# Kernel tuning notes

Hardware: AMD Instinct MI355X
Metric: run time of the kernel (lower is better)

The kernel has to match this reference:

```python
import jax, jax.numpy as jnp
import numpy as np

ZERO = 1e-8
L = 2            # num_gnn_layers
D = 256          # dim_node_features
B = 32           # graphs per batch
NPG = 256        # nodes per graph
N = B * NPG      # total nodes
E = 131072       # edges per edge-type
MAX_TOKENS = 256 # MAX_TOKENS_OF_A_POST
UPD = 0.5        # args.updated_weights_for_A


def _make_edges(k):
    k1, k2, k3 = jax.random.split(k, 3)
    g = jax.random.randint(k1, (E,), 0, B) * NPG          # keep edges within a graph
    src = g + jax.random.randint(k2, (E,), 0, NPG)
    dst = g + jax.random.randint(k3, (E,), 0, NPG)
    return jnp.stack([src, dst]).astype(jnp.int64)


def setup_inputs() -> dict:
    key = jax.random.key(0)
    ks = jax.random.split(key, 12)
    x = jax.random.normal(ks[0], (N, D), dtype=jnp.float32)
    ei_e = _make_edges(ks[1]); ew_e = jax.random.uniform(ks[2], (E,), dtype=jnp.float32)
    ei_p = _make_edges(ks[3]); ew_p = jax.random.uniform(ks[4], (E,), dtype=jnp.float32)
    ei_o = _make_edges(ks[5]); ew_o = jax.random.uniform(ks[6], (E,), dtype=jnp.float32)
    entity_mask = jax.random.randint(ks[7], (B, NPG), 0, 2).astype(bool)
    pattern_mask = jax.random.randint(ks[8], (B, NPG), 0, 2).astype(bool)
    s = 1.0 / np.sqrt(D)
    W_gcn = (jax.random.normal(ks[9], (L, 3, D, D), dtype=jnp.float32) * s)
    b_gcn = jnp.zeros((L, 3, D), dtype=jnp.float32)
    T_dyn = (jax.random.normal(ks[10], (L, D, D), dtype=jnp.float32) * s)
    return {
        'x': x,
        'edge_index_entity': ei_e, 'edge_weight_entity': ew_e,
        'edge_index_pattern': ei_p, 'edge_weight_pattern': ew_p,
        'edge_index_others': ei_o, 'edge_weight_others': ew_o,
        'entity_mask': entity_mask, 'pattern_mask': pattern_mask,
        'W_gcn': W_gcn, 'b_gcn': b_gcn, 'T_dyn': T_dyn,
    }


def _normalized_correlation_matrix(H):
    # cosine-similarity correlation matrix, symmetrically degree-normalized
    nrm = jnp.sqrt(jnp.sum(H * H, axis=1))
    A = (H @ H.T) / (nrm[:, None] * nrm[None, :] + ZERO)
    dinv = 1.0 / jnp.sqrt(jnp.abs(jnp.sum(A, axis=1)) + ZERO)
    return dinv[:, None] * A * dinv[None, :]


def _gcn(H, W, b, ei, ew):
    # GCNConv(add_self_loops=False, normalize=False): scatter-sum of weighted source messages
    msg = (H @ W)[ei[0]] * ew[:, None]                     # [E, D]
    return jax.ops.segment_sum(msg, ei[1], num_segments=N) + b


def _forward(x, we0, wp0, wo0, W_gcn, b_gcn, T_dyn,
             ei_e, ei_p, ei_o, entity_mask, pattern_mask):
    H = x
    A = _normalized_correlation_matrix(H)                  # [N, N]
    for i in range(L):
        if i == 0:
            we, wp, wo = we0, wp0, wo0
        else:
            # diag(one_hot(src) @ A @ one_hot(dst).T) == A[src, dst]
            we = A[ei_e[0], ei_e[1]]
            wp = A[ei_p[0], ei_p[1]]
            wo = A[ei_o[0], ei_o[1]]
        He = _gcn(H, W_gcn[i, 0], b_gcn[i, 0], ei_e, we)
        Hp = _gcn(H, W_gcn[i, 1], b_gcn[i, 1], ei_p, wp)
        Ho = _gcn(H, W_gcn[i, 2], b_gcn[i, 2], ei_o, wo)
        H = jax.nn.relu(He + Hp + Ho)
        A_hat = jax.nn.sigmoid((H @ T_dyn[i]) @ H.T)
        A = (1.0 - UPD) * A + UPD * A_hat
    # per-graph diagonal blocks of A  -> [B, NPG, NPG]
    A4 = A.reshape(B, NPG, B, NPG)
    idx = jnp.arange(B)
    blocks = A4[idx, :, idx, :]
    A_sum = jnp.sum(blocks, axis=-1)                       # [B, NPG]
    ent_cols = jnp.einsum('bij,bj->bi', blocks, entity_mask.astype(A.dtype))
    pat_cols = jnp.einsum('bij,bj->bi', blocks, pattern_mask.astype(A.dtype))
    map_pattern = A_sum - ent_cols
    map_entity = A_sum - pat_cols

    def finish(m):
        mn = jnp.min(m, axis=1, keepdims=True)
        mx = jnp.max(m, axis=1, keepdims=True)
        m = (m - mn) / (mx - mn + ZERO)
        m = m / (jnp.sum(m, axis=1, keepdims=True) + ZERO)
        return m[:, :MAX_TOKENS]                           # padding() with NPG==MAX_TOKENS

    return finish(map_entity), finish(map_pattern)


def reference(x, edge_index_entity, edge_weight_entity,
              edge_index_pattern, edge_weight_pattern,
              edge_index_others, edge_weight_others,
              entity_mask, pattern_mask, W_gcn, b_gcn, T_dyn):
    return _forward(x, edge_weight_entity, edge_weight_pattern, edge_weight_others,
                    W_gcn, b_gcn, T_dyn,
                    edge_index_entity, edge_index_pattern, edge_index_others,
                    entity_mask, pattern_mask)
```

## Files before the change

### kernel.cpp

```cpp
#include <hip/hip_runtime.h>

#define NND   8192
#define DDIM  256
#define NGRP  32
#define ZEROF 1e-8f
#define LSTR  40
#define TSTR  72
#define OFF_AH 0
#define OFF_AL 2560
#define OFF_BH 5120
#define OFF_BL 10240
#define OFF_TT 5120
#define LDS_U16 16384

typedef unsigned short u16;
typedef __attribute__((ext_vector_type(8))) short short8v;
typedef __attribute__((ext_vector_type(4))) float float4v;

__device__ inline u16 f2bf(float x) {
  unsigned u = __float_as_uint(x);
  u += 0x7fffu + ((u >> 16) & 1u);
  return (u16)(u >> 16);
}
__device__ inline float bf2f(u16 h) { return __uint_as_float((unsigned)h << 16); }
__device__ inline void split2(float x, u16& h, u16& l) {
  h = f2bf(x);
  l = f2bf(x - bf2f(h));
}

__device__ inline float wave_sum(float v) {
#pragma unroll
  for (int off = 32; off > 0; off >>= 1) v += __shfl_down(v, off, 64);
  return v;
}

#define LOAD_REGS(tt, kk)                                                                   \
  {                                                                                         \
    int m_ = tid >> 2, kq_ = (tid & 3) * 8;                                                 \
    size_t aoff_;                                                                           \
    if (MODE == 1)                                                                          \
      aoff_ = (size_t)((tt) * 256 + bym * 64 + m_) * 8192 + (size_t)(g * 256 + (kk) + kq_); \
    else if (MODE == 2 || MODE == 3)                                                        \
      aoff_ = (size_t)(g * 256 + bym * 64 + m_) * 256 + (kk) + kq_;                         \
    else                                                                                    \
      aoff_ = (size_t)(bym * 64 + m_) * 256 + (kk) + kq_;                                   \
    rAh = *(const short8v*)&Ah_g[aoff_];                                                    \
    rAl = *(const short8v*)&Al_g[aoff_];                                                    \
    if (MODE == 1) {                                                                        \
      int n_ = tid >> 2, kq2_ = (tid & 3) * 8;                                              \
      const float* pb_ = Bfp + (((size_t)g * 3 + (tt)) << 16) +                             \
                         (size_t)(col0 + n_) * 256 + (kk) + kq2_;                           \
      rBf[0] = *(const float4*)pb_;                                                         \
      rBf[1] = *(const float4*)(pb_ + 4);                                                   \
    } else if (HALF) {                                                                      \
      int n_ = tid & 63, kq2_ = (tid >> 6) * 8;                                             \
      size_t boff_ = (size_t)(((MODE == 2 || MODE == 3) ? g * 256 : 0) + col0 + n_) * 256   \
                     + (kk) + kq2_;                                                         \
      rBh0 = *(const short8v*)&Bh_g[boff_];                                                 \
      rBl0 = *(const short8v*)&Bl_g[boff_];                                                 \
    } else {                                                                                \
      int n_ = tid & 127, kq2_ = (tid >> 7) * 16;                                           \
      size_t boff_ = (size_t)(col0 + n_) * 256 + (kk) + kq2_;                               \
      rBh0 = *(const short8v*)&Bh_g[boff_]; rBh1 = *(const short8v*)&Bh_g[boff_ + 8];       \
      rBl0 = *(const short8v*)&Bl_g[boff_]; rBl1 = *(const short8v*)&Bl_g[boff_ + 8];       \
    }                                                                                       \
  }

template<int MODE, bool HALF>
__device__ __forceinline__ void mfma_body(
    u16* lds,
    const u16* __restrict__ Ah_g, const u16* __restrict__ Al_g,
    const u16* __restrict__ Bh_g, const u16* __restrict__ Bl_g,
    const float* __restrict__ Bfp,
    float* __restrict__ Cf, u16* __restrict__ Ch, u16* __restrict__ Cl,
    const float* __restrict__ nrm, const float* __restrict__ dinv,
    const float* __restrict__ bias,
    int bxm, int bym, int g) {
  u16* Ahs = lds + OFF_AH;
  u16* Als = lds + OFF_AL;
  u16* Bhs = lds + OFF_BH;
  u16* Bls = lds + OFF_BL;
  u16* Tt  = lds + OFF_TT;
  const int NJ = HALF ? 2 : 4;
  const int tid = threadIdx.x;
  const int col0 = bxm * (HALF ? 64 : 128);
  const int w = tid >> 6, lane = tid & 63;
  const int lm = lane & 15, lq = lane >> 4;
  const int wr = (w >> 1) * 32, wc = (w & 1) * (HALF ? 32 : 64);

  float4v acc[2][4];
#pragma unroll
  for (int i = 0; i < 2; ++i)
#pragma unroll
    for (int j = 0; j < NJ; ++j) acc[i][j] = (float4v)0.f;

  short8v rAh, rAl, rBh0, rBh1, rBl0, rBl1;
  float4 rBf[2];
  const int TOTAL = (MODE == 1) ? 24 : 8;

  LOAD_REGS(0, 0);
  for (int step = 0; step < TOTAL; ++step) {
    if (step) __syncthreads();
    {
      int m = tid >> 2, kq = (tid & 3) * 8;
      *(short8v*)&Ahs[m * LSTR + kq] = rAh;
      *(short8v*)&Als[m * LSTR + kq] = rAl;
    }
    if (MODE == 1) {
      int n = tid >> 2, kq2 = (tid & 3) * 8;
      u16 hh[8], ll[8];
      split2(rBf[0].x, hh[0], ll[0]); split2(rBf[0].y, hh[1], ll[1]);
      split2(rBf[0].z, hh[2], ll[2]); split2(rBf[0].w, hh[3], ll[3]);
      split2(rBf[1].x, hh[4], ll[4]); split2(rBf[1].y, hh[5], ll[5]);
      split2(rBf[1].z, hh[6], ll[6]); split2(rBf[1].w, hh[7], ll[7]);
      *(short8v*)&Bhs[n * LSTR + kq2] = *(short8v*)hh;
      *(short8v*)&Bls[n * LSTR + kq2] = *(short8v*)ll;
    } else if (HALF) {
      int n = tid & 63, kq2 = (tid >> 6) * 8;
      *(short8v*)&Bhs[n * LSTR + kq2] = rBh0;
      *(short8v*)&Bls[n * LSTR + kq2] = rBl0;
    } else {
      int n = tid & 127, kq2 = (tid >> 7) * 16;
      *(short8v*)&Bhs[n * LSTR + kq2] = rBh0; *(short8v*)&Bhs[n * LSTR + kq2 + 8] = rBh1;
      *(short8v*)&Bls[n * LSTR + kq2] = rBl0; *(short8v*)&Bls[n * LSTR + kq2 + 8] = rBl1;
    }
    __syncthreads();
    int nxt = step + 1;
    if (nxt < TOTAL) {
      int tt = nxt >> 3, kk = (nxt & 7) * 32;
      LOAD_REGS(tt, kk);
    }
    short8v ah[2], al[2], bh[4], bl[4];
#pragma unroll
    for (int i = 0; i < 2; ++i) {
      int r = wr + i * 16 + lm;
      ah[i] = *(const short8v*)&Ahs[r * LSTR + lq * 8];
      al[i] = *(const short8v*)&Als[r * LSTR + lq * 8];
    }
#pragma unroll
    for (int j = 0; j < NJ; ++j) {
      int r = wc + j * 16 + lm;
      bh[j] = *(const short8v*)&Bhs[r * LSTR + lq * 8];
      bl[j] = *(const short8v*)&Bls[r * LSTR + lq * 8];
    }
#pragma unroll
    for (int i = 0; i < 2; ++i)
#pragma unroll
      for (int j = 0; j < NJ; ++j) {
        acc[i][j] = __builtin_amdgcn_mfma_f32_16x16x32_bf16(ah[i], bh[j], acc[i][j], 0, 0, 0);
        acc[i][j] = __builtin_amdgcn_mfma_f32_16x16x32_bf16(ah[i], bl[j], acc[i][j], 0, 0, 0);
        acc[i][j] = __builtin_amdgcn_mfma_f32_16x16x32_bf16(al[i], bh[j], acc[i][j], 0, 0, 0);
      }
  }

  if (MODE == 2 || MODE == 3) {
#pragma unroll
    for (int i = 0; i < 2; ++i) {
#pragma unroll
      for (int r = 0; r < 4; ++r) {
        int grow = g * 256 + bym * 64 + wr + i * 16 + lq * 4 + r;
        float di = 0.f, ni = 0.f;
        if (MODE == 2) { di = dinv[grow]; ni = nrm[grow]; }
#pragma unroll
        for (int j = 0; j < NJ; ++j) {
          int gcol = col0 + wc + j * 16 + lm;
          size_t ci = (size_t)grow * 256 + gcol;
          float v = acc[i][j][r];
          if (MODE == 2) {
            int gj = g * 256 + gcol;
            Cf[ci] = v * di * dinv[gj] / (ni * nrm[gj] + ZEROF);
          } else {
            Cf[ci] = 0.5f * Cf[ci] + 0.5f * (1.f / (1.f + expf(-v)));
          }
        }
      }
    }
  } else {
    float bsum[8];
    if (MODE == 1) {
#pragma unroll
      for (int i = 0; i < 2; ++i)
#pragma unroll
        for (int r = 0; r < 4; ++r) {
          int d = bym * 64 + wr + i * 16 + lq * 4 + r;
          bsum[i * 4 + r] = bias[d] + bias[256 + d] + bias[512 + d];
        }
    }
    u16 hv[32], lv[32];
#pragma unroll
    for (int i = 0; i < 2; ++i)
#pragma unroll
      for (int j = 0; j < NJ; ++j)
#pragma unroll
        for (int r = 0; r < 4; ++r) {
          float v = acc[i][j][r];
          if (MODE == 1) v = fmaxf(v + bsum[i * 4 + r], 0.f);
          split2(v, hv[(i * 4 + r) * NJ + j], lv[(i * 4 + r) * NJ + j]);
        }
    int ebase1 = (MODE == 1) ? (g * 256 + col0) : col0;
    int ebase2 = bym * 64;
    size_t estride = (MODE == 0) ? 8192 : 256;
#pragma unroll
    for (int ph = 0; ph < 2; ++ph) {
      __syncthreads();
      const u16* sv = ph ? lv : hv;
#pragma unroll
      for (int i = 0; i < 2; ++i)
#pragma unroll
        for (int j = 0; j < NJ; ++j)
#pragma unroll
          for (int r = 0; r < 4; ++r)
            Tt[(wc + j * 16 + lm) * TSTR + wr + i * 16 + lq * 4 + r] = sv[(i * 4 + r) * NJ + j];
      __syncthreads();
      u16* dst = ph ? Cl : Ch;
      int cc0 = tid >> 3, mm0 = (tid & 7) * 8;
#pragma unroll
      for (int it = 0; it < (HALF ? 2 : 4); ++it) {
        int cc = it * 32 + cc0;
        short8v v = *(const short8v*)&Tt[cc * TSTR + mm0];
        *(short8v*)&dst[(size_t)(ebase1 + cc) * estride + ebase2 + mm0] = v;
      }
    }
  }
}

__global__ void k_prep(const int* __restrict__ e0, const int* __restrict__ e1,
                       const int* __restrict__ e2, const unsigned char* __restrict__ m0,
                       const unsigned char* __restrict__ m1,
                       const float* __restrict__ W, const float* __restrict__ T,
                       const float* __restrict__ x,
                       const float* __restrict__ ew0, const float* __restrict__ ew1,
                       const float* __restrict__ ew2,
                       float* __restrict__ emf, float* __restrict__ pmf,
                       u16* __restrict__ Wth, u16* __restrict__ Wtl,
                       u16* __restrict__ sct, uint2* __restrict__ recs,
                       float* __restrict__ nrm, float* __restrict__ Spart,
                       u16* __restrict__ Hh, u16* __restrict__ Hl,
                       int E_, int nCvt, int nBkt) {
  __shared__ float tile[32][33];
  __shared__ float inv[64];
  __shared__ int nz[1];
  __shared__ unsigned int hcnt[768];
  __shared__ unsigned int hoff[768];
  __shared__ unsigned int ppart[256];
  __shared__ uint2 stage[768];
  const int b = blockIdx.x, tid = threadIdx.x;
  if (b < nCvt) {
    if (tid == 0) nz[0] = 0;
    __syncthreads();
    int i4 = tid * 4;
    int c = (m0[i4 + 1] != 0) + (m0[i4 + 2] != 0) + (m0[i4 + 3] != 0);
    if (c) atomicAdd(&nz[0], c);
    __syncthreads();
    int fM = (nz[0] == 0);
    int i = b * 256 + tid;
    if (i < NND) {
      unsigned char v = fM ? m0[4 * i] : m0[i];
      emf[i] = 1.f - (float)(v != 0);
    } else {
      int j = i - NND;
      unsigned char v = fM ? m1[4 * j] : m1[j];
      pmf[j] = 1.f - (float)(v != 0);
    }
  } else if (b < nCvt + nBkt) {
    if (tid == 0) nz[0] = 0;
    hcnt[tid] = 0; hcnt[tid + 256] = 0; hcnt[tid + 512] = 0;
    __syncthreads();
    if (e0[2 * tid + 1] != 0) atomicAdd(&nz[0], 1);
    __syncthreads();
    int fE = (nz[0] == 0);
    int e = (b - nCvt) * 256 + tid;
    bool valid = (e < E_);
    int mybid[3]; unsigned int myrec[3]; float myw[3];
    if (valid) {
#pragma unroll
      for (int t = 0; t < 3; ++t) {
        const int* ei = (t == 0) ? e0 : ((t == 1) ? e1 : e2);
        int src = fE ? ei[2 * e] : ei[e];
        int dst = fE ? ei[2 * (E_ + e)] : ei[E_ + e];
        int g = src >> 8, s = src & 255, d = dst & 255;
        mybid[t] = ((g * 3 + t) << 3) | (d >> 5);
        myrec[t] = (unsigned)(((d & 31) << 8) | s);
        myw[t] = (t == 0 ? ew0 : (t == 1 ? ew1 : ew2))[e];
        atomicAdd(&hcnt[mybid[t]], 1u);
      }
    }
    __syncthreads();
    unsigned c0 = hcnt[3 * tid], c1 = hcnt[3 * tid + 1], c2 = hcnt[3 * tid + 2];
    unsigned tsum = c0 + c1 + c2;
    ppart[tid] = tsum;
    __syncthreads();
    for (int off = 1; off < 256; off <<= 1) {
      unsigned v = (tid >= off) ? ppart[tid - off] : 0u;
      __syncthreads();
      ppart[tid] += v;
      __syncthreads();
    }
    unsigned base = ppart[tid] - tsum;
    hoff[3 * tid] = base;
    hoff[3 * tid + 1] = base + c0;
    hoff[3 * tid + 2] = base + c0 + c1;
    __syncthreads();
#pragma unroll
    for (int k = 0; k < 3; ++k) {
      int bin = tid + k * 256;
      unsigned cc = hcnt[bin]; if (cc > 31u) cc = 31u;
      sct[(size_t)(b - nCvt) * 768 + bin] = (u16)(hoff[bin] | (cc << 11));
    }
    __syncthreads();
    if (valid) {
#pragma unroll
      for (int t = 0; t < 3; ++t) {
        unsigned slot = atomicAdd(&hoff[mybid[t]], 1u);
        stage[slot] = make_uint2(myrec[t], __float_as_uint(myw[t]));
      }
    }
    __syncthreads();
    uint2* dstp = &recs[(size_t)(b - nCvt) * 768];
    dstp[tid] = stage[tid];
    dstp[tid + 256] = stage[tid + 256];
    dstp[tid + 512] = stage[tid + 512];
  } else if (b < nCvt + nBkt + 512) {
    int bb = b - nCvt - nBkt;
    int mat = bb >> 6, rem = bb & 63;
    int k0 = (rem >> 3) * 32, n0 = (rem & 7) * 32;
    const float* src = (mat < 6) ? (W + (size_t)mat * 65536) : (T + (size_t)(mat - 6) * 65536);
    int r = tid >> 3, c4 = (tid & 7) * 4;
    const float4 v = *(const float4*)&src[(size_t)(k0 + r) * 256 + n0 + c4];
    tile[r][c4 + 0] = v.x; tile[r][c4 + 1] = v.y; tile[r][c4 + 2] = v.z; tile[r][c4 + 3] = v.w;
    __syncthreads();
    float o[4] = {tile[c4 + 0][r], tile[c4 + 1][r], tile[c4 + 2][r], tile[c4 + 3][r]};
    u16 hh[4], ll[4];
#pragma unroll
    for (int q = 0; q < 4; ++q) split2(o[q], hh[q], ll[q]);
    size_t off = (size_t)mat * 65536 + (size_t)(n0 + r) * 256 + k0 + c4;
    *(ushort4*)&Wth[off] = *(ushort4*)hh;
    *(ushort4*)&Wtl[off] = *(ushort4*)ll;
  } else {
    int bn = b - nCvt - nBkt - 512;
    int n0 = bn * 64;
    int w = tid >> 6, lane = tid & 63;
    for (int it = 0; it < 16; ++it) {
      int nl = it * 4 + w;
      int node = n0 + nl;
      const float4 v = *(const float4*)&x[(size_t)node * 256 + lane * 4];
      u16 hh[4], ll[4];
      split2(v.x, hh[0], ll[0]); split2(v.y, hh[1], ll[1]);
      split2(v.z, hh[2], ll[2]); split2(v.w, hh[3], ll[3]);
      *(ushort4*)&Hh[(size_t)node * 256 + lane * 4] = *(ushort4*)hh;
      *(ushort4*)&Hl[(size_t)node * 256 + lane * 4] = *(ushort4*)ll;
      float s = wave_sum(v.x * v.x + v.y * v.y + v.z * v.z + v.w * v.w);
      if (lane == 0) { float nr = sqrtf(s); nrm[node] = nr; inv[nl] = 1.f / nr; }
    }
    __syncthreads();
    float s = 0.f;
    for (int i = 0; i < 64; ++i) s += x[(size_t)(n0 + i) * 256 + tid] * inv[i];
    Spart[bn * 256 + tid] = s;
  }
}

__global__ __launch_bounds__(256, 2) void k_stageA(
    const u16* __restrict__ Hinh, const u16* __restrict__ Hinl,
    const u16* __restrict__ Wth, const u16* __restrict__ Wtl, int l,
    u16* __restrict__ XWTh, u16* __restrict__ XWTl,
    const u16* __restrict__ sct, const uint2* __restrict__ recs, int nBkt,
    const float* __restrict__ Abuf, float* __restrict__ Mb,
    const float* __restrict__ x, const float* __restrict__ Spart,
    const float* __restrict__ nrm, float* __restrict__ dinv) {
  __shared__ u16 lds[LDS_U16];
  const int b = blockIdx.x;
  if (b < 768) {
    mfma_body<0, false>(lds, Hinh, Hinl, Wth + (size_t)l * 768 * 256,
                        Wtl + (size_t)l * 768 * 256, nullptr,
                        nullptr, XWTh, XWTl, nullptr, nullptr, nullptr,
                        b >> 7, b & 127, 0);
  } else if (b < 1536) {
    const int tid = threadIdx.x;
    int bid = b - 768;
    int gt = bid >> 3, chunk = bid & 7;
    int g = gt / 3;
    float* tile = (float*)lds;
    float4 z = make_float4(0.f, 0.f, 0.f, 0.f);
#pragma unroll
    for (int k = 0; k < 8; ++k) ((float4*)tile)[k * 256 + tid] = z;
    __syncthreads();
    for (int bb = tid; bb < nBkt; bb += 256) {
      unsigned sc = sct[(size_t)bb * 768 + bid];
      unsigned start = sc & 2047u, cnt = sc >> 11;
      const uint2* rp = &recs[(size_t)bb * 768 + start];
      for (unsigned k = 0; k < cnt; ++k) {
        uint2 r = rp[k];
        int s = r.x & 255, d5 = (r.x >> 8) & 31;
        float w = l ? Abuf[(size_t)(g * 256 + s) * 256 + chunk * 32 + d5]
                    : __uint_as_float(r.y);
        atomicAdd(&tile[d5 * 256 + s], w);
      }
    }
    __syncthreads();
    float4* dst = (float4*)&Mb[((size_t)gt << 16) + ((size_t)chunk << 13)];
#pragma unroll
    for (int k = 0; k < 8; ++k) dst[k * 256 + tid] = ((float4*)tile)[k * 256 + tid];
  } else {
    float* Sl = (float*)lds;
    const int tid = threadIdx.x;
    float s = 0.f;
    for (int bb = 0; bb < 128; ++bb) s += Spart[bb * 256 + tid];
    Sl[tid] = s;
    __syncthreads();
    int base = (b - 1536) * 64;
    int w = tid >> 6, lane = tid & 63;
    const float4 sv = *(const float4*)&Sl[lane * 4];
    for (int it = 0; it < 16; ++it) {
      int node = base + it * 4 + w;
      const float4 v = *(const float4*)&x[(size_t)node * 256 + lane * 4];
      float s2 = wave_sum(v.x * sv.x + v.y * sv.y + v.z * sv.z + v.w * sv.w);
      if (lane == 0) {
        float rowsum = s2 / nrm[node];
        dinv[node] = rsqrtf(fabsf(rowsum) + ZEROF);
      }
    }
  }
}

__global__ __launch_bounds__(256, 2) void k_stageB(
    const u16* __restrict__ XWTh, const u16* __restrict__ XWTl,
    const float* __restrict__ Mb,
    u16* __restrict__ Houth, u16* __restrict__ Houtl, const float* __restrict__ bias,
    const u16* __restrict__ xh, const u16* __restrict__ xl, float* __restrict__ Abuf,
    const float* __restrict__ nrm, const float* __restrict__ dinv) {
  __shared__ u16 lds[LDS_U16];
  const int b = blockIdx.x;
  if (b < 512) {
    int g = b & 31, r = b >> 5;
    mfma_body<1, true>(lds, XWTh, XWTl, nullptr, nullptr, Mb,
                       nullptr, Houth, Houtl, nullptr, nullptr, bias,
                       r >> 2, r & 3, g);
  } else {
    int bb = b - 512;
    int g = bb & 31, r = bb >> 5;
    mfma_body<2, true>(lds, xh, xl, xh, xl, nullptr, Abuf, nullptr, nullptr,
                       nrm, dinv, nullptr, r >> 2, r & 3, g);
  }
}

__global__ __launch_bounds__(256, 2) void k_stageC(
    const u16* __restrict__ Wth, const u16* __restrict__ Wtl, int l,
    const u16* __restrict__ Hh, const u16* __restrict__ Hl,
    u16* __restrict__ tmph, u16* __restrict__ tmpl) {
  __shared__ u16 lds[LDS_U16];
  const int b = blockIdx.x;
  mfma_body<4, true>(lds, Wth + (size_t)(6 + l) * 65536, Wtl + (size_t)(6 + l) * 65536,
                     Hh, Hl, nullptr, nullptr, tmph, tmpl, nullptr, nullptr, nullptr,
                     b & 127, b >> 7, 0);
}

__global__ __launch_bounds__(256, 2) void k_stageD(
    const u16* __restrict__ tmph, const u16* __restrict__ tmpl,
    const u16* __restrict__ Hh, const u16* __restrict__ Hl,
    float* __restrict__ Abuf) {
  __shared__ u16 lds[LDS_U16];
  const int b = blockIdx.x;
  int g = b & 31, r = b >> 5;
  mfma_body<3, true>(lds, tmph, tmpl, Hh, Hl, nullptr, Abuf, nullptr, nullptr,
                     nullptr, nullptr, nullptr, r >> 2, r & 3, g);
}

__global__ void k_maps(const float* __restrict__ Abuf, const float* __restrict__ emf,
                       const float* __restrict__ pmf, float* __restrict__ out) {
  __shared__ float sme[256], smp[256], red[256];
  const int g = blockIdx.x, tid = threadIdx.x, w = tid >> 6, lane = tid & 63;
  const int j0 = g * 256 + lane * 4;
  const float4 pmv = *(const float4*)&pmf[j0];
  const float4 emv = *(const float4*)&emf[j0];
  for (int it = 0; it < 64; ++it) {
    int nl = it * 4 + w;
    const float4 a = *(const float4*)&Abuf[((size_t)g * 256 + nl) * 256 + lane * 4];
    float me = a.x * pmv.x + a.y * pmv.y + a.z * pmv.z + a.w * pmv.w;
    float mp = a.x * emv.x + a.y * emv.y + a.z * emv.z + a.w * emv.w;
#pragma unroll
    for (int off = 32; off > 0; off >>= 1) {
      me += __shfl_down(me, off, 64);
      mp += __shfl_down(mp, off, 64);
    }
    if (lane == 0) { sme[nl] = me; smp[nl] = mp; }
  }
  __syncthreads();
  for (int which = 0; which < 2; ++which) {
    float v = which ? smp[tid] : sme[tid];
    red[tid] = v; __syncthreads();
    for (int s = 128; s > 0; s >>= 1) { if (tid < s) red[tid] = fminf(red[tid], red[tid + s]); __syncthreads(); }
    float mn = red[0]; __syncthreads();
    red[tid] = v; __syncthreads();
    for (int s = 128; s > 0; s >>= 1) { if (tid < s) red[tid] = fmaxf(red[tid], red[tid + s]); __syncthreads(); }
    float mx = red[0]; __syncthreads();
    float m = (v - mn) / (mx - mn + ZEROF);
    red[tid] = m; __syncthreads();
    for (int s = 128; s > 0; s >>= 1) { if (tid < s) red[tid] += red[tid + s]; __syncthreads(); }
    float sum = red[0]; __syncthreads();
    out[which * NND + g * 256 + tid] = m / (sum + ZEROF);
  }
}

extern "C" void kernel_launch(void* const* d_in, const int* in_sizes, int n_in,
                              void* d_out, int out_size, void* d_ws, size_t ws_size,
                              hipStream_t stream) {
  const float* x = (const float*)d_in[0];
  const unsigned char* em_raw = (const unsigned char*)d_in[7];
  const unsigned char* pm_raw = (const unsigned char*)d_in[8];
  const float* W  = (const float*)d_in[9];
  const float* bg = (const float*)d_in[10];
  const float* T  = (const float*)d_in[11];
  float* out = (float*)d_out;
  const int E_ = in_sizes[2];

  const int nCvt = (2 * NND) / 256;
  const int nBkt = (E_ + 255) / 256;

  float* ws = (float*)d_ws;
  size_t o = 0;
  float* Abuf = ws + o; o += (size_t)NND * 256;
  float* Mb3  = ws + o; o += (size_t)2 * NGRP * 3 * 65536;
  u16* Hh   = (u16*)(ws + o); o += (size_t)NND * 256 / 2;
  u16* Hl   = (u16*)(ws + o); o += (size_t)NND * 256 / 2;
  u16* H2h  = (u16*)(ws + o); o += (size_t)NND * 256 / 2;
  u16* H2l  = (u16*)(ws + o); o += (size_t)NND * 256 / 2;
  u16* tmph = (u16*)(ws + o); o += (size_t)NND * 256 / 2;
  u16* tmpl = (u16*)(ws + o); o += (size_t)NND * 256 / 2;
  u16* XWTh = (u16*)(ws + o); o += (size_t)768 * NND / 2;
  u16* XWTl = (u16*)(ws + o); o += (size_t)768 * NND / 2;
  u16* Wth  = (u16*)(ws + o); o += (size_t)8 * 65536 / 2;
  u16* Wtl  = (u16*)(ws + o); o += (size_t)8 * 65536 / 2;
  float* nrm   = ws + o; o += NND;
  float* dinv  = ws + o; o += NND;
  float* Spart = ws + o; o += 128 * 256;
  float* emf   = ws + o; o += NND;
  float* pmf   = ws + o; o += NND;
  u16* sct     = (u16*)(ws + o); o += (size_t)nBkt * 768 / 2;
  uint2* recs  = (uint2*)(ws + o); o += (size_t)nBkt * 768 * 2;

  const float* ew0 = (const float*)d_in[2];
  const float* ew1 = (const float*)d_in[4];
  const float* ew2 = (const float*)d_in[6];
  float* Mb_l0 = Mb3;
  float* Mb_l1 = Mb3 + (size_t)NGRP * 3 * 65536;

  k_prep<<<nCvt + nBkt + 512 + 128, 256, 0, stream>>>(
      (const int*)d_in[1], (const int*)d_in[3], (const int*)d_in[5], em_raw, pm_raw,
      W, T, x, ew0, ew1, ew2, emf, pmf, Wth, Wtl, sct, recs,
      nrm, Spart, Hh, Hl, E_, nCvt, nBkt);

  k_stageA<<<1664, 256, 0, stream>>>(Hh, Hl, Wth, Wtl, 0, XWTh, XWTl,
                                     sct, recs, nBkt, Abuf, Mb_l0,
                                     x, Spart, nrm, dinv);
  k_stageB<<<1024, 256, 0, stream>>>(XWTh, XWTl, Mb_l0, H2h, H2l, bg,
                                     Hh, Hl, Abuf, nrm, dinv);
  k_stageC<<<512, 256, 0, stream>>>(Wth, Wtl, 0, H2h, H2l, tmph, tmpl);
  k_stageD<<<512, 256, 0, stream>>>(tmph, tmpl, H2h, H2l, Abuf);

  k_stageA<<<1536, 256, 0, stream>>>(H2h, H2l, Wth, Wtl, 1, XWTh, XWTl,
                                     sct, recs, nBkt, Abuf, Mb_l1,
                                     x, Spart, nrm, dinv);
  k_stageB<<<512, 256, 0, stream>>>(XWTh, XWTl, Mb_l1, Hh, Hl, bg + 768,
                                    nullptr, nullptr, nullptr, nullptr, nullptr);
  k_stageC<<<512, 256, 0, stream>>>(Wth, Wtl, 1, Hh, Hl, tmph, tmpl);
  k_stageD<<<512, 256, 0, stream>>>(tmph, tmpl, Hh, Hl, Abuf);

  k_maps<<<NGRP, 256, 0, stream>>>(Abuf, emf, pmf, out);
}
```

Measured before the change: 275.3 us.

## Store scatter matrices as bf16 hi/lo split and widen stage-B GEMM tiles

```diff
diff --git a/kernel.cpp b/kernel.cpp
--- a/kernel.cpp
+++ b/kernel.cpp
@@ -46,21 +46,16 @@
       aoff_ = (size_t)(bym * 64 + m_) * 256 + (kk) + kq_;                                   \
     rAh = *(const short8v*)&Ah_g[aoff_];                                                    \
     rAl = *(const short8v*)&Al_g[aoff_];                                                    \
-    if (MODE == 1) {                                                                        \
-      int n_ = tid >> 2, kq2_ = (tid & 3) * 8;                                              \
-      const float* pb_ = Bfp + (((size_t)g * 3 + (tt)) << 16) +                             \
-                         (size_t)(col0 + n_) * 256 + (kk) + kq2_;                           \
-      rBf[0] = *(const float4*)pb_;                                                         \
-      rBf[1] = *(const float4*)(pb_ + 4);                                                   \
-    } else if (HALF) {                                                                      \
+    size_t bbase_ = (MODE == 1) ? ((size_t)(g * 3 + (tt)) << 16)                            \
+                  : ((MODE == 2 || MODE == 3) ? ((size_t)g << 16) : (size_t)0);             \
+    if (HALF) {                                                                             \
       int n_ = tid & 63, kq2_ = (tid >> 6) * 8;                                             \
-      size_t boff_ = (size_t)(((MODE == 2 || MODE == 3) ? g * 256 : 0) + col0 + n_) * 256   \
-                     + (kk) + kq2_;                                                         \
+      size_t boff_ = bbase_ + (size_t)(col0 + n_) * 256 + (kk) + kq2_;                      \
       rBh0 = *(const short8v*)&Bh_g[boff_];                                                 \
       rBl0 = *(const short8v*)&Bl_g[boff_];                                                 \
     } else {                                                                                \
       int n_ = tid & 127, kq2_ = (tid >> 7) * 16;                                           \
-      size_t boff_ = (size_t)(col0 + n_) * 256 + (kk) + kq2_;                               \
+      size_t boff_ = bbase_ + (size_t)(col0 + n_) * 256 + (kk) + kq2_;                      \
       rBh0 = *(const short8v*)&Bh_g[boff_]; rBh1 = *(const short8v*)&Bh_g[boff_ + 8];       \
       rBl0 = *(const short8v*)&Bl_g[boff_]; rBl1 = *(const short8v*)&Bl_g[boff_ + 8];       \
     }                                                                                       \
@@ -71,7 +66,6 @@
     u16* lds,
     const u16* __restrict__ Ah_g, const u16* __restrict__ Al_g,
     const u16* __restrict__ Bh_g, const u16* __restrict__ Bl_g,
-    const float* __restrict__ Bfp,
     float* __restrict__ Cf, u16* __restrict__ Ch, u16* __restrict__ Cl,
     const float* __restrict__ nrm, const float* __restrict__ dinv,
     const float* __restrict__ bias,
@@ -95,7 +89,6 @@
     for (int j = 0; j < NJ; ++j) acc[i][j] = (float4v)0.f;
 
   short8v rAh, rAl, rBh0, rBh1, rBl0, rBl1;
-  float4 rBf[2];
   const int TOTAL = (MODE == 1) ? 24 : 8;
 
   LOAD_REGS(0, 0);
@@ -106,16 +99,7 @@
       *(short8v*)&Ahs[m * LSTR + kq] = rAh;
       *(short8v*)&Als[m * LSTR + kq] = rAl;
     }
-    if (MODE == 1) {
-      int n = tid >> 2, kq2 = (tid & 3) * 8;
-      u16 hh[8], ll[8];
-      split2(rBf[0].x, hh[0], ll[0]); split2(rBf[0].y, hh[1], ll[1]);
-      split2(rBf[0].z, hh[2], ll[2]); split2(rBf[0].w, hh[3], ll[3]);
-      split2(rBf[1].x, hh[4], ll[4]); split2(rBf[1].y, hh[5], ll[5]);
-      split2(rBf[1].z, hh[6], ll[6]); split2(rBf[1].w, hh[7], ll[7]);
-      *(short8v*)&Bhs[n * LSTR + kq2] = *(short8v*)hh;
-      *(short8v*)&Bls[n * LSTR + kq2] = *(short8v*)ll;
-    } else if (HALF) {
+    if (HALF) {
       int n = tid & 63, kq2 = (tid >> 6) * 8;
       *(short8v*)&Bhs[n * LSTR + kq2] = rBh0;
       *(short8v*)&Bls[n * LSTR + kq2] = rBl0;
@@ -359,27 +343,29 @@
   }
 }
 
-__global__ __launch_bounds__(256, 2) void k_stageA(
+__global__ __launch_bounds__(256, 2) void k_gemmA(
     const u16* __restrict__ Hinh, const u16* __restrict__ Hinl,
     const u16* __restrict__ Wth, const u16* __restrict__ Wtl, int l,
-    u16* __restrict__ XWTh, u16* __restrict__ XWTl,
+    u16* __restrict__ XWTh, u16* __restrict__ XWTl) {
+  __shared__ u16 lds[LDS_U16];
+  const int b = blockIdx.x;
+  mfma_body<0, false>(lds, Hinh, Hinl, Wth + (size_t)l * 768 * 256,
+                      Wtl + (size_t)l * 768 * 256,
+                      nullptr, XWTh, XWTl, nullptr, nullptr, nullptr,
+                      b >> 7, b & 127, 0);
+}
+
+__global__ __launch_bounds__(256, 2) void k_mbuild(
     const u16* __restrict__ sct, const uint2* __restrict__ recs, int nBkt,
-    const float* __restrict__ Abuf, float* __restrict__ Mb,
+    const float* __restrict__ Abuf, u16* __restrict__ Mbh, u16* __restrict__ Mbl, int l,
     const float* __restrict__ x, const float* __restrict__ Spart,
     const float* __restrict__ nrm, float* __restrict__ dinv) {
-  __shared__ u16 lds[LDS_U16];
-  const int b = blockIdx.x;
+  __shared__ float tile[8192];
+  const int b = blockIdx.x, tid = threadIdx.x;
   if (b < 768) {
-    mfma_body<0, false>(lds, Hinh, Hinl, Wth + (size_t)l * 768 * 256,
-                        Wtl + (size_t)l * 768 * 256, nullptr,
-                        nullptr, XWTh, XWTl, nullptr, nullptr, nullptr,
-                        b >> 7, b & 127, 0);
-  } else if (b < 1536) {
-    const int tid = threadIdx.x;
-    int bid = b - 768;
+    int bid = b;
     int gt = bid >> 3, chunk = bid & 7;
     int g = gt / 3;
-    float* tile = (float*)lds;
     float4 z = make_float4(0.f, 0.f, 0.f, 0.f);
 #pragma unroll
     for (int k = 0; k < 8; ++k) ((float4*)tile)[k * 256 + tid] = z;
@@ -397,17 +383,23 @@
       }
     }
     __syncthreads();
-    float4* dst = (float4*)&Mb[((size_t)gt << 16) + ((size_t)chunk << 13)];
-#pragma unroll
-    for (int k = 0; k < 8; ++k) dst[k * 256 + tid] = ((float4*)tile)[k * 256 + tid];
+    size_t base4 = ((size_t)gt << 14) + ((size_t)chunk << 11);
+#pragma unroll
+    for (int k = 0; k < 8; ++k) {
+      float4 f = ((float4*)tile)[k * 256 + tid];
+      ushort4 h, lo;
+      split2(f.x, h.x, lo.x); split2(f.y, h.y, lo.y);
+      split2(f.z, h.z, lo.z); split2(f.w, h.w, lo.w);
+      ((ushort4*)Mbh)[base4 + k * 256 + tid] = h;
+      ((ushort4*)Mbl)[base4 + k * 256 + tid] = lo;
+    }
   } else {
-    float* Sl = (float*)lds;
-    const int tid = threadIdx.x;
+    float* Sl = tile;
     float s = 0.f;
     for (int bb = 0; bb < 128; ++bb) s += Spart[bb * 256 + tid];
     Sl[tid] = s;
     __syncthreads();
-    int base = (b - 1536) * 64;
+    int base = (b - 768) * 64;
     int w = tid >> 6, lane = tid & 63;
     const float4 sv = *(const float4*)&Sl[lane * 4];
     for (int it = 0; it < 16; ++it) {
@@ -424,21 +416,21 @@
 
 __global__ __launch_bounds__(256, 2) void k_stageB(
     const u16* __restrict__ XWTh, const u16* __restrict__ XWTl,
-    const float* __restrict__ Mb,
+    const u16* __restrict__ Mbh, const u16* __restrict__ Mbl,
     u16* __restrict__ Houth, u16* __restrict__ Houtl, const float* __restrict__ bias,
     const u16* __restrict__ xh, const u16* __restrict__ xl, float* __restrict__ Abuf,
     const float* __restrict__ nrm, const float* __restrict__ dinv) {
   __shared__ u16 lds[LDS_U16];
   const int b = blockIdx.x;
-  if (b < 512) {
+  if (b < 256) {
     int g = b & 31, r = b >> 5;
-    mfma_body<1, true>(lds, XWTh, XWTl, nullptr, nullptr, Mb,
-                       nullptr, Houth, Houtl, nullptr, nullptr, bias,
-                       r >> 2, r & 3, g);
+    mfma_body<1, false>(lds, XWTh, XWTl, Mbh, Mbl,
+                        nullptr, Houth, Houtl, nullptr, nullptr, bias,
+                        r & 1, r >> 1, g);
   } else {
-    int bb = b - 512;
+    int bb = b - 256;
     int g = bb & 31, r = bb >> 5;
-    mfma_body<2, true>(lds, xh, xl, xh, xl, nullptr, Abuf, nullptr, nullptr,
+    mfma_body<2, true>(lds, xh, xl, xh, xl, Abuf, nullptr, nullptr,
                        nrm, dinv, nullptr, r >> 2, r & 3, g);
   }
 }
@@ -450,7 +442,7 @@
   __shared__ u16 lds[LDS_U16];
   const int b = blockIdx.x;
   mfma_body<4, true>(lds, Wth + (size_t)(6 + l) * 65536, Wtl + (size_t)(6 + l) * 65536,
-                     Hh, Hl, nullptr, nullptr, tmph, tmpl, nullptr, nullptr, nullptr,
+                     Hh, Hl, nullptr, tmph, tmpl, nullptr, nullptr, nullptr,
                      b & 127, b >> 7, 0);
 }
 
@@ -461,7 +453,7 @@
   __shared__ u16 lds[LDS_U16];
   const int b = blockIdx.x;
   int g = b & 31, r = b >> 5;
-  mfma_body<3, true>(lds, tmph, tmpl, Hh, Hl, nullptr, Abuf, nullptr, nullptr,
+  mfma_body<3, true>(lds, tmph, tmpl, Hh, Hl, Abuf, nullptr, nullptr,
                      nullptr, nullptr, nullptr, r >> 2, r & 3, g);
 }
 
@@ -519,7 +511,10 @@
   float* ws = (float*)d_ws;
   size_t o = 0;
   float* Abuf = ws + o; o += (size_t)NND * 256;
-  float* Mb3  = ws + o; o += (size_t)2 * NGRP * 3 * 65536;
+  u16* Mbh_l0 = (u16*)(ws + o); o += (size_t)NGRP * 3 * 65536 / 2;
+  u16* Mbl_l0 = (u16*)(ws + o); o += (size_t)NGRP * 3 * 65536 / 2;
+  u16* Mbh_l1 = (u16*)(ws + o); o += (size_t)NGRP * 3 * 65536 / 2;
+  u16* Mbl_l1 = (u16*)(ws + o); o += (size_t)NGRP * 3 * 65536 / 2;
   u16* Hh   = (u16*)(ws + o); o += (size_t)NND * 256 / 2;
   u16* Hl   = (u16*)(ws + o); o += (size_t)NND * 256 / 2;
   u16* H2h  = (u16*)(ws + o); o += (size_t)NND * 256 / 2;
@@ -541,26 +536,24 @@
   const float* ew0 = (const float*)d_in[2];
   const float* ew1 = (const float*)d_in[4];
   const float* ew2 = (const float*)d_in[6];
-  float* Mb_l0 = Mb3;
-  float* Mb_l1 = Mb3 + (size_t)NGRP * 3 * 65536;
 
   k_prep<<<nCvt + nBkt + 512 + 128, 256, 0, stream>>>(
       (const int*)d_in[1], (const int*)d_in[3], (const int*)d_in[5], em_raw, pm_raw,
       W, T, x, ew0, ew1, ew2, emf, pmf, Wth, Wtl, sct, recs,
       nrm, Spart, Hh, Hl, E_, nCvt, nBkt);
 
-  k_stageA<<<1664, 256, 0, stream>>>(Hh, Hl, Wth, Wtl, 0, XWTh, XWTl,
-                                     sct, recs, nBkt, Abuf, Mb_l0,
-                                     x, Spart, nrm, dinv);
-  k_stageB<<<1024, 256, 0, stream>>>(XWTh, XWTl, Mb_l0, H2h, H2l, bg,
-                                     Hh, Hl, Abuf, nrm, dinv);
+  k_gemmA<<<768, 256, 0, stream>>>(Hh, Hl, Wth, Wtl, 0, XWTh, XWTl);
+  k_mbuild<<<896, 256, 0, stream>>>(sct, recs, nBkt, Abuf, Mbh_l0, Mbl_l0, 0,
+                                    x, Spart, nrm, dinv);
+  k_stageB<<<768, 256, 0, stream>>>(XWTh, XWTl, Mbh_l0, Mbl_l0, H2h, H2l, bg,
+                                    Hh, Hl, Abuf, nrm, dinv);
   k_stageC<<<512, 256, 0, stream>>>(Wth, Wtl, 0, H2h, H2l, tmph, tmpl);
   k_stageD<<<512, 256, 0, stream>>>(tmph, tmpl, H2h, H2l, Abuf);
 
-  k_stageA<<<1536, 256, 0, stream>>>(H2h, H2l, Wth, Wtl, 1, XWTh, XWTl,
-                                     sct, recs, nBkt, Abuf, Mb_l1,
-                                     x, Spart, nrm, dinv);
-  k_stageB<<<512, 256, 0, stream>>>(XWTh, XWTl, Mb_l1, Hh, Hl, bg + 768,
+  k_gemmA<<<768, 256, 0, stream>>>(H2h, H2l, Wth, Wtl, 1, XWTh, XWTl);
+  k_mbuild<<<768, 256, 0, stream>>>(sct, recs, nBkt, Abuf, Mbh_l1, Mbl_l1, 1,
+                                    x, Spart, nrm, dinv);
+  k_stageB<<<256, 256, 0, stream>>>(XWTh, XWTl, Mbh_l1, Mbl_l1, Hh, Hl, bg + 768,
                                     nullptr, nullptr, nullptr, nullptr, nullptr);
   k_stageC<<<512, 256, 0, stream>>>(Wth, Wtl, 1, Hh, Hl, tmph, tmpl);
   k_stageD<<<512, 256, 0, stream>>>(tmph, tmpl, Hh, Hl, Abuf);
```

New measurement: 299.6 us. 8.8% more time.
